# Optimization experiments

Measured on AMD Instinct MI355X. Metric: run time of the kernel, lower is better.

The kernel has to match this reference:

```python
import jax, jax.numpy as jnp
import numpy as np

EXPR_NUM = 80
N_PTS = 2_000_000


def setup_inputs() -> dict:
    key = jax.random.key(0)
    ks = jax.random.split(key, 16)
    L, C = 64, 32
    return {
        "expr": jax.random.normal(ks[0], (EXPR_NUM,), jnp.float32) * 0.1,
        "jaw_quat_weight": jax.random.normal(ks[1], (16, 1), jnp.float32) * 0.1,
        "xyz": jax.random.uniform(ks[2], (N_PTS, 3), jnp.float32),
        "feat_lines_x": jax.random.normal(ks[3], (96, L, C), jnp.float32) * 0.02,
        "feat_lines_y": jax.random.normal(ks[4], (96, L, C), jnp.float32) * 0.02,
        "feat_lines_z": jax.random.normal(ks[5], (96, L, C), jnp.float32) * 0.02,
        "w0_v": jax.random.normal(ks[6], (128, 192), jnp.float32) * (1.0 / np.sqrt(192)),
        "w0_g": jax.random.uniform(ks[7], (128,), jnp.float32, 0.5, 1.5),
        "b0": jax.random.normal(ks[8], (128,), jnp.float32) * 0.01,
        "w1_v": jax.random.normal(ks[9], (128, 128), jnp.float32) * (1.0 / np.sqrt(128)),
        "w1_g": jax.random.uniform(ks[10], (128,), jnp.float32, 0.5, 1.5),
        "b1": jax.random.normal(ks[11], (128,), jnp.float32) * 0.01,
        "w2_v": jax.random.normal(ks[12], (1, 128), jnp.float32) * (1.0 / np.sqrt(128)),
        "w2_g": jax.random.uniform(ks[13], (1,), jnp.float32, 0.5, 1.5),
        "b2": jax.random.normal(ks[14], (1,), jnp.float32) * 0.01,
    }


def _wn_linear(x, v, g, b):
    # weight_norm: W = g * v / ||v||_row (norm over input dim)
    norm = jnp.sqrt(jnp.sum(v * v, axis=1))
    W = v * (g / norm)[:, None]
    return x @ W.T + b


def _sample_line(bs_line, jaw_line, pts):
    # bs_line, jaw_line: [L, C]; pts: [N] in [0,1]
    L = bs_line.shape[0]
    p = jnp.clip(pts, 0.0, 1.0) * (L - 1)
    li = jnp.floor(p).astype(jnp.int32)
    ri = jnp.minimum(li + 1, L - 1)
    w = (p - li.astype(p.dtype))[:, None]
    bs = bs_line[li] + w * (bs_line[ri] - bs_line[li])
    jaw = jaw_line[li] + w * (jaw_line[ri] - jaw_line[li])
    return bs, jaw


def reference(expr, jaw_quat_weight, xyz,
              feat_lines_x, feat_lines_y, feat_lines_z,
              w0_v, w0_g, b0, w1_v, w1_g, b1, w2_v, w2_g, b2):
    e = expr.reshape(-1)[:EXPR_NUM]             # [80]
    jw = jaw_quat_weight.reshape(-1)            # [16] (k=1 broadcast in torch einsum)
    # weighted sums over blendshape / jaw pose lines -> [L, C]
    bs_x = jnp.einsum('ilc,i->lc', feat_lines_x[:EXPR_NUM], e)
    bs_y = jnp.einsum('ilc,i->lc', feat_lines_y[:EXPR_NUM], e)
    bs_z = jnp.einsum('ilc,i->lc', feat_lines_z[:EXPR_NUM], e)
    jaw_x = jnp.einsum('ilc,i->lc', feat_lines_x[EXPR_NUM:], jw)
    jaw_y = jnp.einsum('ilc,i->lc', feat_lines_y[EXPR_NUM:], jw)
    jaw_z = jnp.einsum('ilc,i->lc', feat_lines_z[EXPR_NUM:], jw)
    bx, jx = _sample_line(bs_x, jaw_x, xyz[:, 0])
    by, jy = _sample_line(bs_y, jaw_y, xyz[:, 1])
    bz, jz = _sample_line(bs_z, jaw_z, xyz[:, 2])
    fea = jnp.concatenate((bx, by, bz, jx, jy, jz), axis=1)  # [N, 192]
    fea = jax.nn.relu(_wn_linear(fea, w0_v, w0_g, b0))
    fea = jax.nn.relu(_wn_linear(fea, w1_v, w1_g, b1))
    return _wn_linear(fea, w2_v, w2_g, b2)                   # [N, 1]
```

## Files before the change

kernel.cpp:

```cpp
#include <hip/hip_runtime.h>
#include <math.h>

typedef _Float16 h2 __attribute__((ext_vector_type(2)));
typedef _Float16 f16x8 __attribute__((ext_vector_type(8)));
typedef float f32x4 __attribute__((ext_vector_type(4)));


__global__ void precompute_ws(const float* __restrict__ w0v,
                              const float* __restrict__ w0g,
                              const float* __restrict__ w1v,
                              const float* __restrict__ w1g,
                              const float* __restrict__ w2v,
                              const float* __restrict__ w2g,
                              float* __restrict__ w0scale,
                              float* __restrict__ w2n,
                              h2* __restrict__ Wf) {
    __shared__ float s1[128];
    int t = threadIdx.x;
    if (t < 128) {
        float ns = 0.f;
        for (int c = 0; c < 192; ++c) { float v = w0v[t * 192 + c]; ns += v * v; }
        w0scale[t] = w0g[t] / sqrtf(ns);
        float n1 = 0.f;
        for (int k = 0; k < 128; ++k) { float v = w1v[t * 128 + k]; n1 += v * v; }
        s1[t] = w1g[t] / sqrtf(n1);
        float n2 = 0.f;
        for (int k = 0; k < 128; ++k) { float v = w2v[k]; n2 += v * v; }
        w2n[t] = w2v[t] * (w2g[0] / sqrtf(n2));
    }
    __syncthreads();
    for (int pi = t; pi < 8192; pi += 512) {
        int jp = pi & 3;
        int lane = (pi >> 2) & 63;
        int f = pi >> 8;
        int kk = f >> 3, nt = f & 7;
        int n = nt * 16 + (lane & 15);
        int k = kk * 32 + (lane >> 4) * 8 + jp * 2;
        float s = s1[n];
        h2 v;
        v.x = (_Float16)(w1v[n * 128 + k] * s);
        v.y = (_Float16)(w1v[n * 128 + k + 1] * s);
        Wf[pi] = v;
    }
}

__global__ void precompute_T(const float* __restrict__ expr,
                             const float* __restrict__ jqw,
                             const float* __restrict__ flx,
                             const float* __restrict__ fly,
                             const float* __restrict__ flz,
                             const float* __restrict__ w0v,
                             const float* __restrict__ w0scale,
                             const float* __restrict__ b0,
                             float* __restrict__ T) {
    int a = blockIdx.x >> 6;
    int l = blockIdx.x & 63;
    const float* fl = (a == 0) ? flx : (a == 1) ? fly : flz;
    __shared__ float bs[32];
    __shared__ float jaw[32];
    int t = threadIdx.x;
    if (t < 32) {
        float s = 0.f;
        for (int i = 0; i < 80; ++i) s += expr[i] * fl[(i * 64 + l) * 32 + t];
        bs[t] = s;
    } else if (t < 64) {
        int c = t - 32;
        float s = 0.f;
        for (int i = 0; i < 16; ++i) s += jqw[i] * fl[((80 + i) * 64 + l) * 32 + c];
        jaw[c] = s;
    }
    __syncthreads();
    int j = t;
    float acc = 0.f;
    for (int c = 0; c < 32; ++c) acc += w0v[j * 192 + a * 32 + c] * bs[c];
    for (int c = 0; c < 32; ++c) acc += w0v[j * 192 + 96 + a * 32 + c] * jaw[c];
    acc *= w0scale[j];
    if (a == 0) acc += b0[j];
    T[(a * 64 + l) * 128 + j] = acc;
}

#define T_ROW_CHUNKS 17
#define LDS_T_H2 (192 * T_ROW_CHUNKS * 4)

template <int CTRL>
static __device__ __forceinline__ float dpp_ror_add(float x) {
    int yi = __builtin_amdgcn_update_dpp(0, __builtin_bit_cast(int, x),
                                         CTRL, 0xF, 0xF, false);
    return x + __builtin_bit_cast(float, yi);
}

__launch_bounds__(512)
__attribute__((amdgpu_waves_per_eu(2)))
__global__ void mlp_mfma(const float* __restrict__ xyz,
                         const float* __restrict__ Tg,
                         const f32x4* __restrict__ Wfrag,
                         const float* __restrict__ w2ng,
                         const float* __restrict__ b1,
                         const float* __restrict__ b2p,
                         float* __restrict__ out, int npts) {
    __shared__ __align__(16) h2 tT[LDS_T_H2];
    int tid = threadIdx.x;

    for (int pi = tid; pi < 12288; pi += 512) {
        int r = pi >> 6;
        int p = pi & 63;
        int dst = (r * T_ROW_CHUNKS + (p >> 2)) * 4 + (p & 3);
        h2 v;
        v.x = (_Float16)Tg[2 * pi];
        v.y = (_Float16)Tg[2 * pi + 1];
        tT[dst] = v;
    }
    __syncthreads();

    int lane = tid & 63;
    int lp = lane & 15;
    int lg = lane >> 4;

    f32x4 Bf[4][8];
#pragma unroll
    for (int kk = 0; kk < 4; ++kk)
#pragma unroll
        for (int nt = 0; nt < 8; ++nt)
            Bf[kk][nt] = Wfrag[(((kk * 8 + nt) << 6) | lane)];
#pragma unroll
    for (int kk = 0; kk < 4; ++kk)
#pragma unroll
        for (int nt = 0; nt < 8; ++nt)
            asm volatile("" : "+v"(Bf[kk][nt]));

    float b1r[8], w2r[8];
#pragma unroll
    for (int nt = 0; nt < 8; ++nt) {
        b1r[nt] = b1[nt * 16 + lp];
        w2r[nt] = w2ng[nt * 16 + lp];
    }
    float b2 = b2p[0];

    int waveid = blockIdx.x * 8 + (tid >> 6);
    int nwaves = gridDim.x * 8;
    int ntiles = (npts + 15) >> 4;

#pragma unroll 1
    for (int tile = waveid; tile < ntiles; tile += nwaves) {
        int m0 = tile << 4;
        int p = m0 + lp;
        int pc = min(p, npts - 1);
        float cx = xyz[pc * 3 + 0];
        float cy = xyz[pc * 3 + 1];
        float cz = xyz[pc * 3 + 2];

        f16x8 hA[4];
#pragma unroll
        for (int kk = 0; kk < 4; ++kk)
            hA[kk] = (f16x8){0, 0, 0, 0, 0, 0, 0, 0};

#pragma unroll
        for (int a = 0; a < 3; ++a) {
            float v = (a == 0) ? cx : (a == 1) ? cy : cz;
            v = fminf(fmaxf(v, 0.f), 1.f) * 63.f;
            float fv = floorf(v);
            int li = (int)fv;
            int ri = min(li + 1, 63);
            _Float16 w = (_Float16)(v - fv);
            _Float16 wl = (_Float16)1.0f - w;
            f16x8 w8  = {w, w, w, w, w, w, w, w};
            f16x8 wl8 = {wl, wl, wl, wl, wl, wl, wl, wl};
            int cbL = (a * 64 + li) * T_ROW_CHUNKS;
            int cbR = (a * 64 + ri) * T_ROW_CHUNKS;
#pragma unroll
            for (int kk = 0; kk < 4; ++kk) {
                int cidx = kk * 4 + lg;
                f16x8 vl = *reinterpret_cast<const f16x8*>(&tT[(cbL + cidx) << 2]);
                f16x8 vr = *reinterpret_cast<const f16x8*>(&tT[(cbR + cidx) << 2]);
                hA[kk] = hA[kk] + vl * wl8 + vr * w8;
            }
        }
        f16x8 z8 = (f16x8){0, 0, 0, 0, 0, 0, 0, 0};
#pragma unroll
        for (int kk = 0; kk < 4; ++kk)
            hA[kk] = __builtin_elementwise_max(hA[kk], z8);

        f32x4 acc[8];
#pragma unroll
        for (int nt = 0; nt < 8; ++nt) acc[nt] = (f32x4){0.f, 0.f, 0.f, 0.f};

#pragma unroll
        for (int kk = 0; kk < 4; ++kk) {
#pragma unroll
            for (int nt = 0; nt < 8; ++nt) {
                acc[nt] = __builtin_amdgcn_mfma_f32_16x16x32_f16(
                    hA[kk], __builtin_bit_cast(f16x8, Bf[kk][nt]), acc[nt],
                    0, 0, 0);
            }
        }

        float part0 = 0.f, part1 = 0.f, part2 = 0.f, part3 = 0.f;
#pragma unroll
        for (int nt = 0; nt < 8; ++nt) {
            part0 += w2r[nt] * fmaxf(acc[nt][0] + b1r[nt], 0.f);
            part1 += w2r[nt] * fmaxf(acc[nt][1] + b1r[nt], 0.f);
            part2 += w2r[nt] * fmaxf(acc[nt][2] + b1r[nt], 0.f);
            part3 += w2r[nt] * fmaxf(acc[nt][3] + b1r[nt], 0.f);
        }
        part0 = dpp_ror_add<0x128>(part0);
        part1 = dpp_ror_add<0x128>(part1);
        part2 = dpp_ror_add<0x128>(part2);
        part3 = dpp_ror_add<0x128>(part3);
        part0 = dpp_ror_add<0x124>(part0);
        part1 = dpp_ror_add<0x124>(part1);
        part2 = dpp_ror_add<0x124>(part2);
        part3 = dpp_ror_add<0x124>(part3);
        part0 = dpp_ror_add<0x122>(part0);
        part1 = dpp_ror_add<0x122>(part1);
        part2 = dpp_ror_add<0x122>(part2);
        part3 = dpp_ror_add<0x122>(part3);
        part0 = dpp_ror_add<0x121>(part0);
        part1 = dpp_ror_add<0x121>(part1);
        part2 = dpp_ror_add<0x121>(part2);
        part3 = dpp_ror_add<0x121>(part3);

        int mbase = m0 + (lg << 2);
        if (lp == 0 && mbase + 0 < npts) out[mbase + 0] = part0 + b2;
        if (lp == 1 && mbase + 1 < npts) out[mbase + 1] = part1 + b2;
        if (lp == 2 && mbase + 2 < npts) out[mbase + 2] = part2 + b2;
        if (lp == 3 && mbase + 3 < npts) out[mbase + 3] = part3 + b2;
    }
}

extern "C" void kernel_launch(void* const* d_in, const int* in_sizes, int n_in,
                              void* d_out, int out_size, void* d_ws, size_t ws_size,
                              hipStream_t stream) {
    const float* expr = (const float*)d_in[0];
    const float* jqw  = (const float*)d_in[1];
    const float* xyz  = (const float*)d_in[2];
    const float* flx  = (const float*)d_in[3];
    const float* fly  = (const float*)d_in[4];
    const float* flz  = (const float*)d_in[5];
    const float* w0v  = (const float*)d_in[6];
    const float* w0g  = (const float*)d_in[7];
    const float* b0   = (const float*)d_in[8];
    const float* w1v  = (const float*)d_in[9];
    const float* w1g  = (const float*)d_in[10];
    const float* b1   = (const float*)d_in[11];
    const float* w2v  = (const float*)d_in[12];
    const float* w2g  = (const float*)d_in[13];
    const float* b2   = (const float*)d_in[14];

    float* ws = (float*)d_ws;
    float* T       = ws;
    float* w0scale = ws + 24576;
    float* w2n     = ws + 24704;
    h2*    Wf      = (h2*)(ws + 24832);

    int npts = in_sizes[2] / 3;

    precompute_ws<<<1, 512, 0, stream>>>(w0v, w0g, w1v, w1g, w2v, w2g,
                                         w0scale, w2n, Wf);
    precompute_T<<<192, 128, 0, stream>>>(expr, jqw, flx, fly, flz, w0v,
                                          w0scale, b0, T);
    mlp_mfma<<<256, 512, 0, stream>>>(xyz, T, (const f32x4*)Wf, w2n, b1, b2,
                                      (float*)d_out, npts);
}
```

Baseline: 235.6 us.

## Process two tiles per iteration with software-prefetched coordinates and bias-initialized accumulators

```diff
diff --git a/kernel.cpp b/kernel.cpp
--- a/kernel.cpp
+++ b/kernel.cpp
@@ -139,91 +139,133 @@
     int waveid = blockIdx.x * 8 + (tid >> 6);
     int nwaves = gridDim.x * 8;
     int ntiles = (npts + 15) >> 4;
+    int npairs = (ntiles + 1) >> 1;
+
+    float cc[2][3];
+    {
+        int pr = waveid;
+        int prc = min(pr, npairs - 1);
+#pragma unroll
+        for (int u = 0; u < 2; ++u) {
+            int pc = min(((prc * 2 + u) << 4) + lp, npts - 1);
+            cc[u][0] = xyz[pc * 3 + 0];
+            cc[u][1] = xyz[pc * 3 + 1];
+            cc[u][2] = xyz[pc * 3 + 2];
+        }
+    }
 
 #pragma unroll 1
-    for (int tile = waveid; tile < ntiles; tile += nwaves) {
-        int m0 = tile << 4;
-        int p = m0 + lp;
-        int pc = min(p, npts - 1);
-        float cx = xyz[pc * 3 + 0];
-        float cy = xyz[pc * 3 + 1];
-        float cz = xyz[pc * 3 + 2];
-
-        f16x8 hA[4];
+    for (int pair = waveid; pair < npairs; pair += nwaves) {
+        float nc[2][3];
+        {
+            int pr = min(pair + nwaves, npairs - 1);
+#pragma unroll
+            for (int u = 0; u < 2; ++u) {
+                int pc = min(((pr * 2 + u) << 4) + lp, npts - 1);
+                nc[u][0] = xyz[pc * 3 + 0];
+                nc[u][1] = xyz[pc * 3 + 1];
+                nc[u][2] = xyz[pc * 3 + 2];
+            }
+        }
+
+        f16x8 hA[2][4];
+#pragma unroll
+        for (int u = 0; u < 2; ++u)
+#pragma unroll
+            for (int kk = 0; kk < 4; ++kk)
+                hA[u][kk] = (f16x8){0, 0, 0, 0, 0, 0, 0, 0};
+
+#pragma unroll
+        for (int u = 0; u < 2; ++u) {
+#pragma unroll
+            for (int a = 0; a < 3; ++a) {
+                float v = cc[u][a];
+                v = fminf(fmaxf(v, 0.f), 1.f) * 63.f;
+                float fv = floorf(v);
+                int li = (int)fv;
+                int ri = min(li + 1, 63);
+                _Float16 w = (_Float16)(v - fv);
+                _Float16 wl = (_Float16)1.0f - w;
+                f16x8 w8  = {w, w, w, w, w, w, w, w};
+                f16x8 wl8 = {wl, wl, wl, wl, wl, wl, wl, wl};
+                int cbL = (a * 64 + li) * T_ROW_CHUNKS;
+                int cbR = (a * 64 + ri) * T_ROW_CHUNKS;
+#pragma unroll
+                for (int kk = 0; kk < 4; ++kk) {
+                    int cidx = kk * 4 + lg;
+                    f16x8 vl = *reinterpret_cast<const f16x8*>(&tT[(cbL + cidx) << 2]);
+                    f16x8 vr = *reinterpret_cast<const f16x8*>(&tT[(cbR + cidx) << 2]);
+                    hA[u][kk] = hA[u][kk] + vl * wl8 + vr * w8;
+                }
+            }
+        }
+        f16x8 z8 = (f16x8){0, 0, 0, 0, 0, 0, 0, 0};
+#pragma unroll
+        for (int u = 0; u < 2; ++u)
+#pragma unroll
+            for (int kk = 0; kk < 4; ++kk)
+                hA[u][kk] = __builtin_elementwise_max(hA[u][kk], z8);
+
+        f32x4 acc[2][8];
+#pragma unroll
+        for (int u = 0; u < 2; ++u)
+#pragma unroll
+            for (int nt = 0; nt < 8; ++nt)
+                acc[u][nt] = (f32x4){b1r[nt], b1r[nt], b1r[nt], b1r[nt]};
+
 #pragma unroll
         for (int kk = 0; kk < 4; ++kk)
-            hA[kk] = (f16x8){0, 0, 0, 0, 0, 0, 0, 0};
-
-#pragma unroll
-        for (int a = 0; a < 3; ++a) {
-            float v = (a == 0) ? cx : (a == 1) ? cy : cz;
-            v = fminf(fmaxf(v, 0.f), 1.f) * 63.f;
-            float fv = floorf(v);
-            int li = (int)fv;
-            int ri = min(li + 1, 63);
-            _Float16 w = (_Float16)(v - fv);
-            _Float16 wl = (_Float16)1.0f - w;
-            f16x8 w8  = {w, w, w, w, w, w, w, w};
-            f16x8 wl8 = {wl, wl, wl, wl, wl, wl, wl, wl};
-            int cbL = (a * 64 + li) * T_ROW_CHUNKS;
-            int cbR = (a * 64 + ri) * T_ROW_CHUNKS;
-#pragma unroll
-            for (int kk = 0; kk < 4; ++kk) {
-                int cidx = kk * 4 + lg;
-                f16x8 vl = *reinterpret_cast<const f16x8*>(&tT[(cbL + cidx) << 2]);
-                f16x8 vr = *reinterpret_cast<const f16x8*>(&tT[(cbR + cidx) << 2]);
-                hA[kk] = hA[kk] + vl * wl8 + vr * w8;
-            }
-        }
-        f16x8 z8 = (f16x8){0, 0, 0, 0, 0, 0, 0, 0};
-#pragma unroll
-        for (int kk = 0; kk < 4; ++kk)
-            hA[kk] = __builtin_elementwise_max(hA[kk], z8);
-
-        f32x4 acc[8];
-#pragma unroll
-        for (int nt = 0; nt < 8; ++nt) acc[nt] = (f32x4){0.f, 0.f, 0.f, 0.f};
-
-#pragma unroll
-        for (int kk = 0; kk < 4; ++kk) {
 #pragma unroll
             for (int nt = 0; nt < 8; ++nt) {
-                acc[nt] = __builtin_amdgcn_mfma_f32_16x16x32_f16(
-                    hA[kk], __builtin_bit_cast(f16x8, Bf[kk][nt]), acc[nt],
-                    0, 0, 0);
-            }
-        }
-
-        float part0 = 0.f, part1 = 0.f, part2 = 0.f, part3 = 0.f;
-#pragma unroll
-        for (int nt = 0; nt < 8; ++nt) {
-            part0 += w2r[nt] * fmaxf(acc[nt][0] + b1r[nt], 0.f);
-            part1 += w2r[nt] * fmaxf(acc[nt][1] + b1r[nt], 0.f);
-            part2 += w2r[nt] * fmaxf(acc[nt][2] + b1r[nt], 0.f);
-            part3 += w2r[nt] * fmaxf(acc[nt][3] + b1r[nt], 0.f);
-        }
-        part0 = dpp_ror_add<0x128>(part0);
-        part1 = dpp_ror_add<0x128>(part1);
-        part2 = dpp_ror_add<0x128>(part2);
-        part3 = dpp_ror_add<0x128>(part3);
-        part0 = dpp_ror_add<0x124>(part0);
-        part1 = dpp_ror_add<0x124>(part1);
-        part2 = dpp_ror_add<0x124>(part2);
-        part3 = dpp_ror_add<0x124>(part3);
-        part0 = dpp_ror_add<0x122>(part0);
-        part1 = dpp_ror_add<0x122>(part1);
-        part2 = dpp_ror_add<0x122>(part2);
-        part3 = dpp_ror_add<0x122>(part3);
-        part0 = dpp_ror_add<0x121>(part0);
-        part1 = dpp_ror_add<0x121>(part1);
-        part2 = dpp_ror_add<0x121>(part2);
-        part3 = dpp_ror_add<0x121>(part3);
-
-        int mbase = m0 + (lg << 2);
-        if (lp == 0 && mbase + 0 < npts) out[mbase + 0] = part0 + b2;
-        if (lp == 1 && mbase + 1 < npts) out[mbase + 1] = part1 + b2;
-        if (lp == 2 && mbase + 2 < npts) out[mbase + 2] = part2 + b2;
-        if (lp == 3 && mbase + 3 < npts) out[mbase + 3] = part3 + b2;
+                acc[0][nt] = __builtin_amdgcn_mfma_f32_16x16x32_f16(
+                    hA[0][kk], __builtin_bit_cast(f16x8, Bf[kk][nt]), acc[0][nt], 0, 0, 0);
+                acc[1][nt] = __builtin_amdgcn_mfma_f32_16x16x32_f16(
+                    hA[1][kk], __builtin_bit_cast(f16x8, Bf[kk][nt]), acc[1][nt], 0, 0, 0);
+            }
+
+#pragma unroll
+        for (int u = 0; u < 2; ++u) {
+            int tile = pair * 2 + u;
+            float part0 = 0.f, part1 = 0.f, part2 = 0.f, part3 = 0.f;
+#pragma unroll
+            for (int nt = 0; nt < 8; ++nt) {
+                part0 += w2r[nt] * fmaxf(acc[u][nt][0], 0.f);
+                part1 += w2r[nt] * fmaxf(acc[u][nt][1], 0.f);
+                part2 += w2r[nt] * fmaxf(acc[u][nt][2], 0.f);
+                part3 += w2r[nt] * fmaxf(acc[u][nt][3], 0.f);
+            }
+            part0 = dpp_ror_add<0x128>(part0);
+            part1 = dpp_ror_add<0x128>(part1);
+            part2 = dpp_ror_add<0x128>(part2);
+            part3 = dpp_ror_add<0x128>(part3);
+            part0 = dpp_ror_add<0x124>(part0);
+            part1 = dpp_ror_add<0x124>(part1);
+            part2 = dpp_ror_add<0x124>(part2);
+            part3 = dpp_ror_add<0x124>(part3);
+            part0 = dpp_ror_add<0x122>(part0);
+            part1 = dpp_ror_add<0x122>(part1);
+            part2 = dpp_ror_add<0x122>(part2);
+            part3 = dpp_ror_add<0x122>(part3);
+            part0 = dpp_ror_add<0x121>(part0);
+            part1 = dpp_ror_add<0x121>(part1);
+            part2 = dpp_ror_add<0x121>(part2);
+            part3 = dpp_ror_add<0x121>(part3);
+
+            if (tile < ntiles) {
+                int mbase = (tile << 4) + (lg << 2);
+                if (lp == 0 && mbase + 0 < npts) out[mbase + 0] = part0 + b2;
+                if (lp == 1 && mbase + 1 < npts) out[mbase + 1] = part1 + b2;
+                if (lp == 2 && mbase + 2 < npts) out[mbase + 2] = part2 + b2;
+                if (lp == 3 && mbase + 3 < npts) out[mbase + 3] = part3 + b2;
+            }
+        }
+
+#pragma unroll
+        for (int u = 0; u < 2; ++u) {
+            cc[u][0] = nc[u][0];
+            cc[u][1] = nc[u][1];
+            cc[u][2] = nc[u][2];
+        }
     }
 }
 
```

Result: slower. 266.4 us (+13.1%).

## Store interleaved line value and delta in LDS, prefetch next tile coordinates

Applied to the files above, without the earlier changes.

```diff
diff --git a/kernel.cpp b/kernel.cpp
--- a/kernel.cpp
+++ b/kernel.cpp
@@ -79,8 +79,8 @@
     T[(a * 64 + l) * 128 + j] = acc;
 }
 
-#define T_ROW_CHUNKS 17
-#define LDS_T_H2 (192 * T_ROW_CHUNKS * 4)
+#define U_ROW_CHUNKS 33
+#define LDS_U_H2 (192 * U_ROW_CHUNKS * 4)
 
 template <int CTRL>
 static __device__ __forceinline__ float dpp_ror_add(float x) {
@@ -98,17 +98,24 @@
                          const float* __restrict__ b1,
                          const float* __restrict__ b2p,
                          float* __restrict__ out, int npts) {
-    __shared__ __align__(16) h2 tT[LDS_T_H2];
+    __shared__ __align__(16) h2 tT[LDS_U_H2];
     int tid = threadIdx.x;
 
-    for (int pi = tid; pi < 12288; pi += 512) {
-        int r = pi >> 6;
-        int p = pi & 63;
-        int dst = (r * T_ROW_CHUNKS + (p >> 2)) * 4 + (p & 3);
-        h2 v;
-        v.x = (_Float16)Tg[2 * pi];
-        v.y = (_Float16)Tg[2 * pi + 1];
-        tT[dst] = v;
+    for (int u = tid; u < 12288; u += 512) {
+        int r = u >> 6;
+        int p = u & 63;
+        int rl = r & 63;
+        float t0 = Tg[2 * u], t1 = Tg[2 * u + 1];
+        float d0 = 0.f, d1 = 0.f;
+        if (rl != 63) {
+            d0 = Tg[2 * u + 128] - t0;
+            d1 = Tg[2 * u + 129] - t1;
+        }
+        int base = (r * U_ROW_CHUNKS + 2 * (p >> 2)) * 4 + (p & 3);
+        h2 tv; tv.x = (_Float16)t0; tv.y = (_Float16)t1;
+        h2 dv; dv.x = (_Float16)d0; dv.y = (_Float16)d1;
+        tT[base] = tv;
+        tT[base + 4] = dv;
     }
     __syncthreads();
 
@@ -140,39 +147,44 @@
     int nwaves = gridDim.x * 8;
     int ntiles = (npts + 15) >> 4;
 
+    float cx, cy, cz;
+    {
+        int pc = min((min(waveid, ntiles - 1) << 4) + lp, npts - 1);
+        cx = xyz[pc * 3 + 0];
+        cy = xyz[pc * 3 + 1];
+        cz = xyz[pc * 3 + 2];
+    }
+
 #pragma unroll 1
     for (int tile = waveid; tile < ntiles; tile += nwaves) {
-        int m0 = tile << 4;
-        int p = m0 + lp;
-        int pc = min(p, npts - 1);
-        float cx = xyz[pc * 3 + 0];
-        float cy = xyz[pc * 3 + 1];
-        float cz = xyz[pc * 3 + 2];
+        float nx, ny, nz;
+        {
+            int pr = min(tile + nwaves, ntiles - 1);
+            int pc = min((pr << 4) + lp, npts - 1);
+            nx = xyz[pc * 3 + 0];
+            ny = xyz[pc * 3 + 1];
+            nz = xyz[pc * 3 + 2];
+        }
 
         f16x8 hA[4];
-#pragma unroll
-        for (int kk = 0; kk < 4; ++kk)
-            hA[kk] = (f16x8){0, 0, 0, 0, 0, 0, 0, 0};
-
 #pragma unroll
         for (int a = 0; a < 3; ++a) {
             float v = (a == 0) ? cx : (a == 1) ? cy : cz;
             v = fminf(fmaxf(v, 0.f), 1.f) * 63.f;
             float fv = floorf(v);
             int li = (int)fv;
-            int ri = min(li + 1, 63);
             _Float16 w = (_Float16)(v - fv);
-            _Float16 wl = (_Float16)1.0f - w;
-            f16x8 w8  = {w, w, w, w, w, w, w, w};
-            f16x8 wl8 = {wl, wl, wl, wl, wl, wl, wl, wl};
-            int cbL = (a * 64 + li) * T_ROW_CHUNKS;
-            int cbR = (a * 64 + ri) * T_ROW_CHUNKS;
+            f16x8 w8 = {w, w, w, w, w, w, w, w};
+            int Rb = (a * 64 + li) * U_ROW_CHUNKS;
 #pragma unroll
             for (int kk = 0; kk < 4; ++kk) {
-                int cidx = kk * 4 + lg;
-                f16x8 vl = *reinterpret_cast<const f16x8*>(&tT[(cbL + cidx) << 2]);
-                f16x8 vr = *reinterpret_cast<const f16x8*>(&tT[(cbR + cidx) << 2]);
-                hA[kk] = hA[kk] + vl * wl8 + vr * w8;
+                int ci = Rb + 2 * (kk * 4 + lg);
+                f16x8 t8 = *reinterpret_cast<const f16x8*>(&tT[ci * 4]);
+                f16x8 d8 = *reinterpret_cast<const f16x8*>(&tT[ci * 4 + 4]);
+                if (a == 0)
+                    hA[kk] = t8 + w8 * d8;
+                else
+                    hA[kk] = hA[kk] + (t8 + w8 * d8);
             }
         }
         f16x8 z8 = (f16x8){0, 0, 0, 0, 0, 0, 0, 0};
@@ -182,25 +194,23 @@
 
         f32x4 acc[8];
 #pragma unroll
-        for (int nt = 0; nt < 8; ++nt) acc[nt] = (f32x4){0.f, 0.f, 0.f, 0.f};
-
-#pragma unroll
-        for (int kk = 0; kk < 4; ++kk) {
-#pragma unroll
-            for (int nt = 0; nt < 8; ++nt) {
+        for (int nt = 0; nt < 8; ++nt)
+            acc[nt] = (f32x4){b1r[nt], b1r[nt], b1r[nt], b1r[nt]};
+
+#pragma unroll
+        for (int kk = 0; kk < 4; ++kk)
+#pragma unroll
+            for (int nt = 0; nt < 8; ++nt)
                 acc[nt] = __builtin_amdgcn_mfma_f32_16x16x32_f16(
-                    hA[kk], __builtin_bit_cast(f16x8, Bf[kk][nt]), acc[nt],
-                    0, 0, 0);
-            }
-        }
+                    hA[kk], __builtin_bit_cast(f16x8, Bf[kk][nt]), acc[nt], 0, 0, 0);
 
         float part0 = 0.f, part1 = 0.f, part2 = 0.f, part3 = 0.f;
 #pragma unroll
         for (int nt = 0; nt < 8; ++nt) {
-            part0 += w2r[nt] * fmaxf(acc[nt][0] + b1r[nt], 0.f);
-            part1 += w2r[nt] * fmaxf(acc[nt][1] + b1r[nt], 0.f);
-            part2 += w2r[nt] * fmaxf(acc[nt][2] + b1r[nt], 0.f);
-            part3 += w2r[nt] * fmaxf(acc[nt][3] + b1r[nt], 0.f);
+            part0 += w2r[nt] * fmaxf(acc[nt][0], 0.f);
+            part1 += w2r[nt] * fmaxf(acc[nt][1], 0.f);
+            part2 += w2r[nt] * fmaxf(acc[nt][2], 0.f);
+            part3 += w2r[nt] * fmaxf(acc[nt][3], 0.f);
         }
         part0 = dpp_ror_add<0x128>(part0);
         part1 = dpp_ror_add<0x128>(part1);
@@ -219,11 +229,14 @@
         part2 = dpp_ror_add<0x121>(part2);
         part3 = dpp_ror_add<0x121>(part3);
 
-        int mbase = m0 + (lg << 2);
-        if (lp == 0 && mbase + 0 < npts) out[mbase + 0] = part0 + b2;
-        if (lp == 1 && mbase + 1 < npts) out[mbase + 1] = part1 + b2;
-        if (lp == 2 && mbase + 2 < npts) out[mbase + 2] = part2 + b2;
-        if (lp == 3 && mbase + 3 < npts) out[mbase + 3] = part3 + b2;
+        float sel = part3;
+        sel = (lp == 2) ? part2 : sel;
+        sel = (lp == 1) ? part1 : sel;
+        sel = (lp == 0) ? part0 : sel;
+        int mi = (tile << 4) + (lg << 2) + lp;
+        if (lp < 4 && mi < npts) out[mi] = sel + b2;
+
+        cx = nx; cy = ny; cz = nz;
     }
 }
 
```

After: 218.2 us. 1.08x faster.
